# Kernel tuning notes

Hardware: AMD Instinct MI355X
Metric: run time of the kernel (lower is better)

The kernel has to match this reference:

```python
import jax, jax.numpy as jnp
import numpy as np

D = 128   # hidden_size
L = 50    # mailbox length (USER_MAX_LEN / ITEM_MAX_LEN)
NU = 8192 # num user nodes
NI = 8192 # num item nodes


def setup_inputs() -> dict:
    key = jax.random.key(0)
    ks = jax.random.split(key, 16)
    s = 0.05
    return {
        "user": jax.random.normal(ks[0], (NU, D), jnp.float32),
        "item": jax.random.normal(ks[1], (NI, D), jnp.float32),
        "W_user": jax.random.normal(ks[2], (D, D), jnp.float32) * s,
        "W_item": jax.random.normal(ks[3], (D, D), jnp.float32) * s,
        "agg_gate_user": jax.random.normal(ks[4], (2 * D, D), jnp.float32) * s,
        "agg_gate_item": jax.random.normal(ks[5], (2 * D, D), jnp.float32) * s,
        "update_user": jax.random.normal(ks[6], (2 * D, D), jnp.float32) * s,
        "update_item": jax.random.normal(ks[7], (2 * D, D), jnp.float32) * s,
        "user_date_emb": jax.random.normal(ks[8], (L, D), jnp.float32) * s,
        "user_date_emb_k": jax.random.normal(ks[9], (L, D), jnp.float32) * s,
        "item_date_emb": jax.random.normal(ks[10], (L, D), jnp.float32) * s,
        "item_date_emb_k": jax.random.normal(ks[11], (L, D), jnp.float32) * s,
        "user_nbr": jax.random.randint(ks[12], (NU, L), 0, NI, jnp.int64) if jax.config.jax_enable_x64 else jax.random.randint(ks[12], (NU, L), 0, NI, jnp.int32),
        "user_nbr_time": jax.random.randint(ks[13], (NU, L), 0, 1000000, jnp.int32),
        "item_nbr": jax.random.randint(ks[14], (NI, L), 0, NU, jnp.int32),
        "item_nbr_time": jax.random.randint(ks[15], (NI, L), 0, 1000000, jnp.int32),
    }


def _reduce(dst_h, src_mail, time, emb, emb_k, gate_W):
    # dst_h: [N,d], src_mail: [N,L,d], time: [N,L]
    # double argsort -> rank; reorder = L - rank - 1 (time-order position)
    order = jnp.argsort(jnp.argsort(time, axis=1), axis=1)
    reorder = time.shape[1] - order - 1                     # [N,L]
    scale = 1.0 / jnp.sqrt(jnp.asarray(dst_h.shape[-1], dst_h.dtype))
    # long-term attention with positional injection
    e = jnp.sum((emb[reorder] + src_mail) * dst_h[:, None, :], axis=-1) * scale
    alpha = jax.nn.softmax(e, axis=1)                       # [N,L]
    h_long = jnp.einsum('nl,nld->nd', alpha, src_mail + emb_k[reorder])
    # short-term attention against most-recent neighbor
    last = jnp.argmax(time, axis=1)                         # [N]
    last_emb = jnp.take_along_axis(src_mail, last[:, None, None], axis=1)  # [N,1,d]
    e1 = jnp.sum(last_emb * src_mail, axis=-1) * scale
    alpha1 = jax.nn.softmax(e1, axis=1)
    h_short = jnp.einsum('nl,nld->nd', alpha1, src_mail)
    return jnp.concatenate([h_long, h_short], axis=-1) @ gate_W  # [N,d]


def reference(user, item, W_user, W_item, agg_gate_user, agg_gate_item,
              update_user, update_item, user_date_emb, user_date_emb_k,
              item_date_emb, item_date_emb_k, user_nbr, user_nbr_time,
              item_nbr, item_nbr_time):
    # feat_drop/attn_drop are identity (eval mode)
    uh = user @ W_user   # [NU,d]
    ih = item @ W_item   # [NI,d]
    # user nodes aggregate item-neighbor mailboxes
    user_agg = _reduce(uh, ih[user_nbr], user_nbr_time,
                       user_date_emb, user_date_emb_k, agg_gate_user)
    # item nodes aggregate user-neighbor mailboxes
    item_agg = _reduce(ih, uh[item_nbr], item_nbr_time,
                       item_date_emb, item_date_emb_k, agg_gate_item)
    user_out = jnp.tanh(jnp.concatenate([user_agg, user], axis=-1) @ update_user)
    item_out = jnp.tanh(jnp.concatenate([item_agg, item], axis=-1) @ update_item)
    return user_out, item_out
```

## Files before the change

### kernel.cpp

```cpp
#include <hip/hip_runtime.h>
#include <math.h>

#define D 128
#define L 50
#define SCALE 0.08838834764831845f

using bf16x8 = __attribute__((ext_vector_type(8))) short;
using f32x4  = __attribute__((ext_vector_type(4))) float;

union FragU { bf16x8 f; uint2 u2[2]; uint4 u4; };

__device__ __forceinline__ unsigned f2bf(float x) {
    union { float f; unsigned u; } v; v.f = x;
    return (v.u + 0x7fffu + ((v.u >> 16) & 1u)) >> 16;
}
__device__ __forceinline__ float bflo(unsigned u) {
    union { unsigned u; float f; } v; v.u = u << 16; return v.f;
}
__device__ __forceinline__ float bfhi(unsigned u) {
    union { unsigned u; float f; } v; v.u = u & 0xffff0000u; return v.f;
}

__global__ __launch_bounds__(256) void prep_all_kernel(
    const float* __restrict__ Wu, const float* __restrict__ Wi,
    const float* __restrict__ ue, const float* __restrict__ ie,
    const float* __restrict__ gu, const float* __restrict__ gi,
    const float* __restrict__ uu, const float* __restrict__ ui,
    const float* __restrict__ uek, const float* __restrict__ iek,
    unsigned short* __restrict__ Bptu, unsigned short* __restrict__ Bpti,
    unsigned short* __restrict__ Btu, unsigned short* __restrict__ Bti)
{
    __shared__ float T[2][128];
    int b = blockIdx.x, t = threadIdx.x;
    if (b < 50) {
        int side = b / 25;
        int o = (b % 25) * 256 + t;
        int d = o / L, l = o % L;
        const float* W = side ? Wi : Wu;
        const float* E = side ? ie : ue;
        unsigned short* Bpt = side ? Bpti : Bptu;
        float a = 0.f;
        for (int k = 0; k < D; ++k) a += W[d * D + k] * E[l * D + k];
        Bpt[(128 + l) * 128 + d] = (unsigned short)f2bf(a);
    } else if (b < 306) {
        int bb = b - 50;
        int side = bb / 128;
        int o = (bb % 128) * 256 + t;
        int r = o >> 7, c = o & 127;
        const float* G = side ? gi : gu;
        const float* U = side ? ui : uu;
        unsigned short* Bt = side ? Bti : Btu;
        float a = 0.f;
        for (int k = 0; k < D; ++k) a += G[r * D + k] * U[k * D + c];
        Bt[c * 448 + r] = (unsigned short)f2bf(a);
    } else if (b < 434) {
        int bb = b - 306;
        int side = bb >> 6;
        int o = (bb & 63) * 256 + t;
        int r = o >> 7, c = o & 127;
        const float* U = side ? ui : uu;
        unsigned short* Bt = side ? Bti : Btu;
        Bt[c * 448 + 320 + r] = (unsigned short)f2bf(U[(128 + r) * D + c]);
        if (r < 14) Bt[c * 448 + 306 + r] = 0;
    } else if (b < 562) {
        int bb = b - 434;
        int side = bb >> 6;
        int o = (bb & 63) * 256 + t;
        int k = o >> 7, c = o & 127;
        const float* W = side ? Wi : Wu;
        unsigned short* Bpt = side ? Bpti : Bptu;
        Bpt[c * 128 + k] = (unsigned short)f2bf(W[k * D + c]);
    } else if (b < 564) {
        int side = b - 562;
        unsigned short* Bpt = side ? Bpti : Bptu;
        for (int j = 0; j < 7; ++j)
            Bpt[178 * 128 + t * 7 + j] = 0;
    } else {
        int bb = b - 564;
        int side = bb / 25;
        int ro = (bb % 25) * 2;
        const float* EK = side ? iek : uek;
        const float* G  = side ? gi : gu;
        const float* U  = side ? ui : uu;
        unsigned short* Bt = side ? Bti : Btu;
        int r = t >> 7, c = t & 127;
        float a = 0.f;
        for (int k = 0; k < D; ++k) a += EK[(ro + r) * D + k] * G[k * D + c];
        T[r][c] = a;
        __syncthreads();
        float e = 0.f;
        for (int j = 0; j < D; ++j) e += T[r][j] * U[j * D + c];
        Bt[c * 448 + 256 + ro + r] = (unsigned short)f2bf(e);
    }
}

__global__ __launch_bounds__(256) void proj_mfma(
    const float* __restrict__ Xu, const float* __restrict__ Xi,
    const unsigned* __restrict__ Bptu32, const unsigned* __restrict__ Bpti32,
    unsigned* __restrict__ h32, float* __restrict__ eproj,
    unsigned* __restrict__ A32, int NU)
{
    __shared__ __align__(16) unsigned Bs[192 * 68];
    int t = threadIdx.x;
    int nb = blockIdx.x * 32;
    const float* X = (nb < NU) ? Xu : Xi;
    int xoff = (nb < NU) ? 0 : NU;
    const unsigned* Bt = (nb < NU) ? Bptu32 : Bpti32;
    int wave = t >> 6, lane = t & 63;
    int m16 = lane & 15, quad = lane >> 4;

    #pragma unroll
    for (int i = 0; i < 12; ++i) {
        int idx = t + i * 256;
        int c = idx >> 4, q = idx & 15;
        uint4 v = *(const uint4*)&Bt[(size_t)c * 64 + q * 4];
        *(uint4*)&Bs[c * 68 + q * 4] = v;
    }
    __syncthreads();

    f32x4 acc[2][3];
    for (int i = 0; i < 2; ++i)
        for (int j = 0; j < 3; ++j) acc[i][j] = (f32x4){0.f, 0.f, 0.f, 0.f};

    #pragma unroll
    for (int kc = 0; kc < 4; ++kc) {
        FragU a[2];
        #pragma unroll
        for (int mi = 0; mi < 2; ++mi) {
            int row = nb + mi * 16 + m16;
            const float* src = &X[(size_t)(row - xoff) * D + kc * 32 + quad * 8];
            float4 v0 = *(const float4*)&src[0];
            float4 v1 = *(const float4*)&src[4];
            uint4 pk;
            pk.x = f2bf(v0.x) | (f2bf(v0.y) << 16);
            pk.y = f2bf(v0.z) | (f2bf(v0.w) << 16);
            pk.z = f2bf(v1.x) | (f2bf(v1.y) << 16);
            pk.w = f2bf(v1.z) | (f2bf(v1.w) << 16);
            a[mi].u4 = pk;
            if (wave == 0)
                *(uint4*)&A32[(size_t)row * 224 + 160 + kc * 16 + quad * 4] = pk;
        }
        #pragma unroll
        for (int ni = 0; ni < 3; ++ni) {
            bf16x8 bb = *(const bf16x8*)&Bs[(wave * 48 + ni * 16 + m16) * 68 + kc * 16 + quad * 4];
            acc[0][ni] = __builtin_amdgcn_mfma_f32_16x16x32_bf16(a[0].f, bb, acc[0][ni], 0, 0, 0);
            acc[1][ni] = __builtin_amdgcn_mfma_f32_16x16x32_bf16(a[1].f, bb, acc[1][ni], 0, 0, 0);
        }
    }
    #pragma unroll
    for (int mi = 0; mi < 2; ++mi)
        #pragma unroll
        for (int ni = 0; ni < 3; ++ni) {
            int col = wave * 48 + ni * 16 + m16;
            #pragma unroll
            for (int r = 0; r < 4; ++r) {
                float me = acc[mi][ni][r];
                float pr = __shfl_xor(me, 1);
                int row = nb + mi * 16 + quad * 4 + r;
                if (col < 128) {
                    if (!(lane & 1))
                        h32[(size_t)row * 64 + (col >> 1)] = f2bf(me) | (f2bf(pr) << 16);
                } else if (col < 178) {
                    eproj[(size_t)row * L + (col - 128)] = me;
                }
            }
        }
}

__global__ __launch_bounds__(256) void agg_kernel(
    const unsigned* __restrict__ h32, const float* __restrict__ eproj,
    const int* __restrict__ unbr, const int* __restrict__ untime,
    const int* __restrict__ inbr, const int* __restrict__ intime,
    unsigned* __restrict__ A32, int NU, int NI)
{
    __shared__ unsigned smail[2][L * 66];
    __shared__ unsigned shb[2][64];
    __shared__ float se2[2][2][64];
    __shared__ float salpha[2][L], salpha1[2][L];
    __shared__ int stime[2][L], sreorder[2][L], snbr[2][L], slast[2];

    int tb = threadIdx.x;
    int sub = tb >> 7;
    int t = tb & 127;
    int g = blockIdx.x * 2 + sub;
    int wave = t >> 6, lane = t & 63;
    int m16 = lane & 15, quad = lane >> 4;

    const unsigned* mail; const int* nbrp; const int* timp;
    if (g < NU) { mail = h32 + (size_t)NU * 64; nbrp = unbr + (size_t)g * L;        timp = untime + (size_t)g * L; }
    else        { mail = h32;                   nbrp = inbr + (size_t)(g - NU) * L; timp = intime + (size_t)(g - NU) * L; }

    if (t < 64) shb[sub][t] = h32[(size_t)g * 64 + t];
    if (t < L) { stime[sub][t] = timp[t]; snbr[sub][t] = nbrp[t]; }
    __syncthreads();

    if (t < L) {
        int ti = stime[sub][t]; int rank = 0; bool firstmax = true;
        for (int j = 0; j < L; ++j) {
            int tj = stime[sub][j];
            rank += (tj < ti) || (tj == ti && j < t);
            firstmax = firstmax && ((tj < ti) || (tj == ti && j >= t));
        }
        sreorder[sub][t] = L - 1 - rank;
        if (firstmax) slast[sub] = t;
    }
    {
        int q = t >> 5, p = t & 31;
        #pragma unroll
        for (int i = 0; i < 13; ++i) {
            int l = i * 4 + q;
            if (l < L) {
                uint2 v = *(const uint2*)&mail[(size_t)snbr[sub][l] * 64 + p * 2];
                *(uint2*)&smail[sub][l * 66 + 2 * p] = v;
            }
        }
    }
    __syncthreads();

    {
        const unsigned* bptr = (m16 == 1) ? &smail[sub][slast[sub] * 66]
                                          : &shb[sub][0];
        int s0 = wave * 32 + m16;  if (s0 > 49) s0 = 49;
        int s1 = wave * 32 + 16 + m16;  if (s1 > 49) s1 = 49;
        const unsigned* a0p = &smail[sub][s0 * 66];
        const unsigned* a1p = &smail[sub][s1 * 66];
        f32x4 d0 = {0.f, 0.f, 0.f, 0.f}, d1 = {0.f, 0.f, 0.f, 0.f};
        #pragma unroll
        for (int kc = 0; kc < 4; ++kc) {
            int off = kc * 16 + quad * 4;
            FragU bf_, af0, af1;
            bf_.u2[0] = *(const uint2*)&bptr[off];
            bf_.u2[1] = *(const uint2*)&bptr[off + 2];
            af0.u2[0] = *(const uint2*)&a0p[off];
            af0.u2[1] = *(const uint2*)&a0p[off + 2];
            af1.u2[0] = *(const uint2*)&a1p[off];
            af1.u2[1] = *(const uint2*)&a1p[off + 2];
            d0 = __builtin_amdgcn_mfma_f32_16x16x32_bf16(af0.f, bf_.f, d0, 0, 0, 0);
            d1 = __builtin_amdgcn_mfma_f32_16x16x32_bf16(af1.f, bf_.f, d1, 0, 0, 0);
        }
        if (m16 < 2) {
            #pragma unroll
            for (int r = 0; r < 4; ++r) {
                se2[sub][m16][wave * 32 + quad * 4 + r]      = d0[r];
                se2[sub][m16][wave * 32 + 16 + quad * 4 + r] = d1[r];
            }
        }
    }
    __syncthreads();

    float sc = -1e30f;
    if (lane < L) {
        sc = (wave == 0)
           ? (se2[sub][0][lane] + eproj[(size_t)g * L + sreorder[sub][lane]]) * SCALE
           : se2[sub][1][lane] * SCALE;
    }
    float mx = sc;
    for (int off = 32; off; off >>= 1) mx = fmaxf(mx, __shfl_xor(mx, off));
    float ex = (lane < L) ? expf(sc - mx) : 0.f;
    float sm = ex;
    for (int off = 32; off; off >>= 1) sm += __shfl_xor(sm, off);
    float al = ex / sm;
    if (lane < L) { if (wave == 0) salpha[sub][lane] = al; else salpha1[sub][lane] = al; }
    __syncthreads();

    {
        const float* alp = wave ? salpha1[sub] : salpha[sub];
        const unsigned* base = &smail[sub][lane];
        float ax = 0.f, ay = 0.f;
        for (int l = 0; l < L; ++l) {
            unsigned u = base[l * 66];
            float a = alp[l];
            ax += a * bflo(u);
            ay += a * bfhi(u);
        }
        A32[(size_t)g * 224 + wave * 64 + lane] = f2bf(ax) | (f2bf(ay) << 16);
    }
    if (t >= 64 && t < 96) A32[(size_t)g * 224 + 128 + (t - 64)] = 0u;
    __syncthreads();
    if (t < L) {
        ((unsigned short*)A32)[(size_t)g * 448 + 256 + sreorder[sub][t]] =
            (unsigned short)f2bf(salpha[sub][t]);
    }
}

__global__ __launch_bounds__(256) void gemm_out_mfma(
    const unsigned* __restrict__ A32,
    const unsigned* __restrict__ Btu32, const unsigned* __restrict__ Bti32,
    float* __restrict__ out, int NU)
{
    __shared__ __align__(16) unsigned Bs[64 * 228];
    int t = threadIdx.x;
    int rowblk = blockIdx.x >> 1, half = blockIdx.x & 1;
    int nb = rowblk * 128;
    const unsigned* Bt = (nb < NU) ? Btu32 : Bti32;
    int wave = t >> 6, lane = t & 63;
    int m16 = lane & 15, quad = lane >> 4;

    #pragma unroll
    for (int i = 0; i < 14; ++i) {
        int idx = t + i * 256;
        int n = idx / 56, q = idx - n * 56;
        uint4 v = *(const uint4*)&Bt[(size_t)(half * 64 + n) * 224 + q * 4];
        *(uint4*)&Bs[n * 228 + q * 4] = v;
    }
    __syncthreads();

    #pragma unroll
    for (int j = 0; j < 2; ++j) {
        int mrow0 = nb + (wave * 2 + j) * 16;
        f32x4 acc[4] = {{0.f,0.f,0.f,0.f},{0.f,0.f,0.f,0.f},
                        {0.f,0.f,0.f,0.f},{0.f,0.f,0.f,0.f}};
        for (int kc = 0; kc < 14; ++kc) {
            FragU af;
            af.u4 = *(const uint4*)&A32[(size_t)(mrow0 + m16) * 224 + kc * 16 + quad * 4];
            #pragma unroll
            for (int ni = 0; ni < 4; ++ni) {
                bf16x8 bf = *(const bf16x8*)&Bs[(ni * 16 + m16) * 228 + kc * 16 + quad * 4];
                acc[ni] = __builtin_amdgcn_mfma_f32_16x16x32_bf16(af.f, bf, acc[ni], 0, 0, 0);
            }
        }
        #pragma unroll
        for (int ni = 0; ni < 4; ++ni)
            #pragma unroll
            for (int r = 0; r < 4; ++r) {
                int row = mrow0 + quad * 4 + r;
                int col = half * 64 + ni * 16 + m16;
                out[(size_t)row * D + col] = tanhf(acc[ni][r]);
            }
    }
}

extern "C" void kernel_launch(void* const* d_in, const int* in_sizes, int n_in,
                              void* d_out, int out_size, void* d_ws, size_t ws_size,
                              hipStream_t stream) {
    const float* user   = (const float*)d_in[0];
    const float* item   = (const float*)d_in[1];
    const float* Wu     = (const float*)d_in[2];
    const float* Wi     = (const float*)d_in[3];
    const float* gate_u = (const float*)d_in[4];
    const float* gate_i = (const float*)d_in[5];
    const float* upd_u  = (const float*)d_in[6];
    const float* upd_i  = (const float*)d_in[7];
    const float* uemb   = (const float*)d_in[8];
    const float* uembk  = (const float*)d_in[9];
    const float* iemb   = (const float*)d_in[10];
    const float* iembk  = (const float*)d_in[11];
    const int*   unbr   = (const int*)d_in[12];
    const int*   untime = (const int*)d_in[13];
    const int*   inbr   = (const int*)d_in[14];
    const int*   intime = (const int*)d_in[15];

    int NU = in_sizes[0] / D;
    int NI = in_sizes[1] / D;
    int N  = NU + NI;

    float* eproj  = (float*)d_ws;
    unsigned* h32   = (unsigned*)(eproj + (size_t)N * L);
    unsigned* A32   = h32 + (size_t)N * 64;
    unsigned* Btu32 = A32 + (size_t)N * 224;
    unsigned* Bti32 = Btu32 + 128 * 224;
    unsigned* Bptu32 = Bti32 + 128 * 224;
    unsigned* Bpti32 = Bptu32 + 192 * 64;

    prep_all_kernel<<<614, 256, 0, stream>>>(Wu, Wi, uemb, iemb, gate_u, gate_i,
                                             upd_u, upd_i, uembk, iembk,
                                             (unsigned short*)Bptu32,
                                             (unsigned short*)Bpti32,
                                             (unsigned short*)Btu32,
                                             (unsigned short*)Bti32);
    proj_mfma<<<N / 32, 256, 0, stream>>>(user, item, Bptu32, Bpti32,
                                          h32, eproj, A32, NU);
    agg_kernel<<<N / 2, 256, 0, stream>>>(h32, eproj, unbr, untime, inbr,
                                          intime, A32, NU, NI);
    gemm_out_mfma<<<N / 64, 256, 0, stream>>>(A32, Btu32, Bti32,
                                              (float*)d_out, NU);
}
```

Baseline: 172.1 us.

## Fuse four stages into one persistent cooperative kernel with grid syncs

Merges the prep, projection, aggregation and output-GEMM kernels into a single persistent cooperative kernel. Blocks loop over work items and a grid.sync separates each stage, which removes three kernel launches and the gaps between them. The projection and output GEMM no longer stage B in shared memory and read it directly from global memory/cache. The projection tile is also halved to 16 rows per work item. Grid size is capped at 768 blocks, which limits parallelism in the agg stage. Host-side attribute and occupancy queries now run on every call, and the old four-kernel path is kept as a fallback.

```diff
diff --git a/kernel.cpp b/kernel.cpp
--- a/kernel.cpp
+++ b/kernel.cpp
@@ -1,5 +1,8 @@
 #include <hip/hip_runtime.h>
+#include <hip/hip_cooperative_groups.h>
 #include <math.h>
+
+namespace cg = cooperative_groups;
 
 #define D 128
 #define L 50
@@ -21,24 +24,31 @@
     union { unsigned u; float f; } v; v.u = u & 0xffff0000u; return v.f;
 }
 
-__global__ __launch_bounds__(256) void prep_all_kernel(
-    const float* __restrict__ Wu, const float* __restrict__ Wi,
-    const float* __restrict__ ue, const float* __restrict__ ie,
-    const float* __restrict__ gu, const float* __restrict__ gi,
-    const float* __restrict__ uu, const float* __restrict__ ui,
-    const float* __restrict__ uek, const float* __restrict__ iek,
-    unsigned short* __restrict__ Bptu, unsigned short* __restrict__ Bpti,
-    unsigned short* __restrict__ Btu, unsigned short* __restrict__ Bti)
-{
-    __shared__ float T[2][128];
-    int b = blockIdx.x, t = threadIdx.x;
+struct AggShared {
+    unsigned smail[2][L * 66];
+    unsigned shb[2][64];
+    float se2[2][2][64];
+    float salpha[2][L], salpha1[2][L];
+    int stime[2][L], sreorder[2][L], snbr[2][L], slast[2];
+};
+struct PrepShared { float T[2][128]; };
+union SharedAll { AggShared agg; PrepShared prep; };
+
+__device__ __forceinline__ void prep_body(
+    int b, int t,
+    const float* Wu, const float* Wi, const float* ue, const float* ie,
+    const float* gu, const float* gi, const float* uu, const float* ui,
+    const float* uek, const float* iek,
+    unsigned* Bptu32, unsigned* Bpti32, unsigned* Btu32, unsigned* Bti32,
+    float T[2][128])
+{
     if (b < 50) {
         int side = b / 25;
         int o = (b % 25) * 256 + t;
         int d = o / L, l = o % L;
         const float* W = side ? Wi : Wu;
         const float* E = side ? ie : ue;
-        unsigned short* Bpt = side ? Bpti : Bptu;
+        unsigned short* Bpt = (unsigned short*)(side ? Bpti32 : Bptu32);
         float a = 0.f;
         for (int k = 0; k < D; ++k) a += W[d * D + k] * E[l * D + k];
         Bpt[(128 + l) * 128 + d] = (unsigned short)f2bf(a);
@@ -49,7 +59,7 @@
         int r = o >> 7, c = o & 127;
         const float* G = side ? gi : gu;
         const float* U = side ? ui : uu;
-        unsigned short* Bt = side ? Bti : Btu;
+        unsigned short* Bt = (unsigned short*)(side ? Bti32 : Btu32);
         float a = 0.f;
         for (int k = 0; k < D; ++k) a += G[r * D + k] * U[k * D + c];
         Bt[c * 448 + r] = (unsigned short)f2bf(a);
@@ -59,7 +69,7 @@
         int o = (bb & 63) * 256 + t;
         int r = o >> 7, c = o & 127;
         const float* U = side ? ui : uu;
-        unsigned short* Bt = side ? Bti : Btu;
+        unsigned short* Bt = (unsigned short*)(side ? Bti32 : Btu32);
         Bt[c * 448 + 320 + r] = (unsigned short)f2bf(U[(128 + r) * D + c]);
         if (r < 14) Bt[c * 448 + 306 + r] = 0;
     } else if (b < 562) {
@@ -68,11 +78,11 @@
         int o = (bb & 63) * 256 + t;
         int k = o >> 7, c = o & 127;
         const float* W = side ? Wi : Wu;
-        unsigned short* Bpt = side ? Bpti : Bptu;
+        unsigned short* Bpt = (unsigned short*)(side ? Bpti32 : Bptu32);
         Bpt[c * 128 + k] = (unsigned short)f2bf(W[k * D + c]);
     } else if (b < 564) {
         int side = b - 562;
-        unsigned short* Bpt = side ? Bpti : Bptu;
+        unsigned short* Bpt = (unsigned short*)(side ? Bpti32 : Bptu32);
         for (int j = 0; j < 7; ++j)
             Bpt[178 * 128 + t * 7 + j] = 0;
     } else {
@@ -82,7 +92,7 @@
         const float* EK = side ? iek : uek;
         const float* G  = side ? gi : gu;
         const float* U  = side ? ui : uu;
-        unsigned short* Bt = side ? Bti : Btu;
+        unsigned short* Bt = (unsigned short*)(side ? Bti32 : Btu32);
         int r = t >> 7, c = t & 127;
         float a = 0.f;
         for (int k = 0; k < D; ++k) a += EK[(ro + r) * D + k] * G[k * D + c];
@@ -91,143 +101,116 @@
         float e = 0.f;
         for (int j = 0; j < D; ++j) e += T[r][j] * U[j * D + c];
         Bt[c * 448 + 256 + ro + r] = (unsigned short)f2bf(e);
-    }
-}
-
-__global__ __launch_bounds__(256) void proj_mfma(
-    const float* __restrict__ Xu, const float* __restrict__ Xi,
-    const unsigned* __restrict__ Bptu32, const unsigned* __restrict__ Bpti32,
-    unsigned* __restrict__ h32, float* __restrict__ eproj,
-    unsigned* __restrict__ A32, int NU)
-{
-    __shared__ __align__(16) unsigned Bs[192 * 68];
-    int t = threadIdx.x;
-    int nb = blockIdx.x * 32;
-    const float* X = (nb < NU) ? Xu : Xi;
+        __syncthreads();
+    }
+}
+
+__device__ __forceinline__ void proj_body(
+    int w, int t, const float* user, const float* item,
+    const unsigned* Bptu32, const unsigned* Bpti32,
+    unsigned* h32, float* eproj, unsigned* A32, int NU)
+{
+    int wave = t >> 6, lane = t & 63;
+    int m16 = lane & 15, quad = lane >> 4;
+    int nb = w * 16;
+    const float* X = (nb < NU) ? user : item;
     int xoff = (nb < NU) ? 0 : NU;
     const unsigned* Bt = (nb < NU) ? Bptu32 : Bpti32;
-    int wave = t >> 6, lane = t & 63;
-    int m16 = lane & 15, quad = lane >> 4;
-
-    #pragma unroll
-    for (int i = 0; i < 12; ++i) {
-        int idx = t + i * 256;
-        int c = idx >> 4, q = idx & 15;
-        uint4 v = *(const uint4*)&Bt[(size_t)c * 64 + q * 4];
-        *(uint4*)&Bs[c * 68 + q * 4] = v;
-    }
-    __syncthreads();
-
-    f32x4 acc[2][3];
-    for (int i = 0; i < 2; ++i)
-        for (int j = 0; j < 3; ++j) acc[i][j] = (f32x4){0.f, 0.f, 0.f, 0.f};
-
+
+    f32x4 acc[3] = {{0.f,0.f,0.f,0.f},{0.f,0.f,0.f,0.f},{0.f,0.f,0.f,0.f}};
     #pragma unroll
     for (int kc = 0; kc < 4; ++kc) {
-        FragU a[2];
-        #pragma unroll
-        for (int mi = 0; mi < 2; ++mi) {
-            int row = nb + mi * 16 + m16;
-            const float* src = &X[(size_t)(row - xoff) * D + kc * 32 + quad * 8];
-            float4 v0 = *(const float4*)&src[0];
-            float4 v1 = *(const float4*)&src[4];
-            uint4 pk;
-            pk.x = f2bf(v0.x) | (f2bf(v0.y) << 16);
-            pk.y = f2bf(v0.z) | (f2bf(v0.w) << 16);
-            pk.z = f2bf(v1.x) | (f2bf(v1.y) << 16);
-            pk.w = f2bf(v1.z) | (f2bf(v1.w) << 16);
-            a[mi].u4 = pk;
-            if (wave == 0)
-                *(uint4*)&A32[(size_t)row * 224 + 160 + kc * 16 + quad * 4] = pk;
-        }
+        int row = nb + m16;
+        const float* src = &X[(size_t)(row - xoff) * D + kc * 32 + quad * 8];
+        float4 v0 = *(const float4*)&src[0];
+        float4 v1 = *(const float4*)&src[4];
+        FragU a;
+        a.u4.x = f2bf(v0.x) | (f2bf(v0.y) << 16);
+        a.u4.y = f2bf(v0.z) | (f2bf(v0.w) << 16);
+        a.u4.z = f2bf(v1.x) | (f2bf(v1.y) << 16);
+        a.u4.w = f2bf(v1.z) | (f2bf(v1.w) << 16);
+        if (wave == 0)
+            *(uint4*)&A32[(size_t)row * 224 + 160 + kc * 16 + quad * 4] = a.u4;
         #pragma unroll
         for (int ni = 0; ni < 3; ++ni) {
-            bf16x8 bb = *(const bf16x8*)&Bs[(wave * 48 + ni * 16 + m16) * 68 + kc * 16 + quad * 4];
-            acc[0][ni] = __builtin_amdgcn_mfma_f32_16x16x32_bf16(a[0].f, bb, acc[0][ni], 0, 0, 0);
-            acc[1][ni] = __builtin_amdgcn_mfma_f32_16x16x32_bf16(a[1].f, bb, acc[1][ni], 0, 0, 0);
+            int c = wave * 48 + ni * 16 + m16;
+            FragU bb;
+            bb.u4 = *(const uint4*)&Bt[(size_t)c * 64 + kc * 16 + quad * 4];
+            acc[ni] = __builtin_amdgcn_mfma_f32_16x16x32_bf16(a.f, bb.f, acc[ni], 0, 0, 0);
         }
     }
     #pragma unroll
-    for (int mi = 0; mi < 2; ++mi)
-        #pragma unroll
-        for (int ni = 0; ni < 3; ++ni) {
-            int col = wave * 48 + ni * 16 + m16;
-            #pragma unroll
-            for (int r = 0; r < 4; ++r) {
-                float me = acc[mi][ni][r];
-                float pr = __shfl_xor(me, 1);
-                int row = nb + mi * 16 + quad * 4 + r;
-                if (col < 128) {
-                    if (!(lane & 1))
-                        h32[(size_t)row * 64 + (col >> 1)] = f2bf(me) | (f2bf(pr) << 16);
-                } else if (col < 178) {
-                    eproj[(size_t)row * L + (col - 128)] = me;
-                }
+    for (int ni = 0; ni < 3; ++ni) {
+        int col = wave * 48 + ni * 16 + m16;
+        #pragma unroll
+        for (int r = 0; r < 4; ++r) {
+            float me = acc[ni][r];
+            float pr = __shfl_xor(me, 1);
+            int row = nb + quad * 4 + r;
+            if (col < 128) {
+                if (!(lane & 1))
+                    h32[(size_t)row * 64 + (col >> 1)] = f2bf(me) | (f2bf(pr) << 16);
+            } else if (col < 178) {
+                eproj[(size_t)row * L + (col - 128)] = me;
             }
         }
-}
-
-__global__ __launch_bounds__(256) void agg_kernel(
-    const unsigned* __restrict__ h32, const float* __restrict__ eproj,
-    const int* __restrict__ unbr, const int* __restrict__ untime,
-    const int* __restrict__ inbr, const int* __restrict__ intime,
-    unsigned* __restrict__ A32, int NU, int NI)
-{
-    __shared__ unsigned smail[2][L * 66];
-    __shared__ unsigned shb[2][64];
-    __shared__ float se2[2][2][64];
-    __shared__ float salpha[2][L], salpha1[2][L];
-    __shared__ int stime[2][L], sreorder[2][L], snbr[2][L], slast[2];
-
-    int tb = threadIdx.x;
+    }
+}
+
+__device__ __forceinline__ void agg_body(
+    int w, int tb, AggShared& sh,
+    const unsigned* h32, const float* eproj,
+    const int* unbr, const int* untime, const int* inbr, const int* intime,
+    unsigned* A32, int NU)
+{
     int sub = tb >> 7;
-    int t = tb & 127;
-    int g = blockIdx.x * 2 + sub;
-    int wave = t >> 6, lane = t & 63;
-    int m16 = lane & 15, quad = lane >> 4;
+    int ta = tb & 127;
+    int awave = ta >> 6, alane = ta & 63;
+    int am16 = alane & 15, aquad = alane >> 4;
+    int g = w * 2 + sub;
 
     const unsigned* mail; const int* nbrp; const int* timp;
     if (g < NU) { mail = h32 + (size_t)NU * 64; nbrp = unbr + (size_t)g * L;        timp = untime + (size_t)g * L; }
     else        { mail = h32;                   nbrp = inbr + (size_t)(g - NU) * L; timp = intime + (size_t)(g - NU) * L; }
 
-    if (t < 64) shb[sub][t] = h32[(size_t)g * 64 + t];
-    if (t < L) { stime[sub][t] = timp[t]; snbr[sub][t] = nbrp[t]; }
-    __syncthreads();
-
-    if (t < L) {
-        int ti = stime[sub][t]; int rank = 0; bool firstmax = true;
+    if (ta < 64) sh.shb[sub][ta] = h32[(size_t)g * 64 + ta];
+    if (ta < L) { sh.stime[sub][ta] = timp[ta]; sh.snbr[sub][ta] = nbrp[ta]; }
+    __syncthreads();
+
+    if (ta < L) {
+        int ti = sh.stime[sub][ta]; int rank = 0; bool firstmax = true;
         for (int j = 0; j < L; ++j) {
-            int tj = stime[sub][j];
-            rank += (tj < ti) || (tj == ti && j < t);
-            firstmax = firstmax && ((tj < ti) || (tj == ti && j >= t));
-        }
-        sreorder[sub][t] = L - 1 - rank;
-        if (firstmax) slast[sub] = t;
+            int tj = sh.stime[sub][j];
+            rank += (tj < ti) || (tj == ti && j < ta);
+            firstmax = firstmax && ((tj < ti) || (tj == ti && j >= ta));
+        }
+        sh.sreorder[sub][ta] = L - 1 - rank;
+        if (firstmax) sh.slast[sub] = ta;
     }
     {
-        int q = t >> 5, p = t & 31;
+        int q = ta >> 5, p = ta & 31;
         #pragma unroll
         for (int i = 0; i < 13; ++i) {
             int l = i * 4 + q;
             if (l < L) {
-                uint2 v = *(const uint2*)&mail[(size_t)snbr[sub][l] * 64 + p * 2];
-                *(uint2*)&smail[sub][l * 66 + 2 * p] = v;
+                uint2 v = *(const uint2*)&mail[(size_t)sh.snbr[sub][l] * 64 + p * 2];
+                *(uint2*)&sh.smail[sub][l * 66 + 2 * p] = v;
             }
         }
     }
     __syncthreads();
 
     {
-        const unsigned* bptr = (m16 == 1) ? &smail[sub][slast[sub] * 66]
-                                          : &shb[sub][0];
-        int s0 = wave * 32 + m16;  if (s0 > 49) s0 = 49;
-        int s1 = wave * 32 + 16 + m16;  if (s1 > 49) s1 = 49;
-        const unsigned* a0p = &smail[sub][s0 * 66];
-        const unsigned* a1p = &smail[sub][s1 * 66];
+        const unsigned* bptr = (am16 == 1) ? &sh.smail[sub][sh.slast[sub] * 66]
+                                           : &sh.shb[sub][0];
+        int s0 = awave * 32 + am16;       if (s0 > 49) s0 = 49;
+        int s1 = awave * 32 + 16 + am16;  if (s1 > 49) s1 = 49;
+        const unsigned* a0p = &sh.smail[sub][s0 * 66];
+        const unsigned* a1p = &sh.smail[sub][s1 * 66];
         f32x4 d0 = {0.f, 0.f, 0.f, 0.f}, d1 = {0.f, 0.f, 0.f, 0.f};
         #pragma unroll
         for (int kc = 0; kc < 4; ++kc) {
-            int off = kc * 16 + quad * 4;
+            int off = kc * 16 + aquad * 4;
             FragU bf_, af0, af1;
             bf_.u2[0] = *(const uint2*)&bptr[off];
             bf_.u2[1] = *(const uint2*)&bptr[off + 2];
@@ -238,34 +221,37 @@
             d0 = __builtin_amdgcn_mfma_f32_16x16x32_bf16(af0.f, bf_.f, d0, 0, 0, 0);
             d1 = __builtin_amdgcn_mfma_f32_16x16x32_bf16(af1.f, bf_.f, d1, 0, 0, 0);
         }
-        if (m16 < 2) {
+        if (am16 < 2) {
             #pragma unroll
             for (int r = 0; r < 4; ++r) {
-                se2[sub][m16][wave * 32 + quad * 4 + r]      = d0[r];
-                se2[sub][m16][wave * 32 + 16 + quad * 4 + r] = d1[r];
+                sh.se2[sub][am16][awave * 32 + aquad * 4 + r]      = d0[r];
+                sh.se2[sub][am16][awave * 32 + 16 + aquad * 4 + r] = d1[r];
             }
         }
     }
     __syncthreads();
 
     float sc = -1e30f;
-    if (lane < L) {
-        sc = (wave == 0)
-           ? (se2[sub][0][lane] + eproj[(size_t)g * L + sreorder[sub][lane]]) * SCALE
-           : se2[sub][1][lane] * SCALE;
+    if (alane < L) {
+        sc = (awave == 0)
+           ? (sh.se2[sub][0][alane] + eproj[(size_t)g * L + sh.sreorder[sub][alane]]) * SCALE
+           : sh.se2[sub][1][alane] * SCALE;
     }
     float mx = sc;
     for (int off = 32; off; off >>= 1) mx = fmaxf(mx, __shfl_xor(mx, off));
-    float ex = (lane < L) ? expf(sc - mx) : 0.f;
-    float sm = ex;
-    for (int off = 32; off; off >>= 1) sm += __shfl_xor(sm, off);
-    float al = ex / sm;
-    if (lane < L) { if (wave == 0) salpha[sub][lane] = al; else salpha1[sub][lane] = al; }
+    float ex = (alane < L) ? expf(sc - mx) : 0.f;
+    float smv = ex;
+    for (int off = 32; off; off >>= 1) smv += __shfl_xor(smv, off);
+    float al = ex / smv;
+    if (alane < L) {
+        if (awave == 0) sh.salpha[sub][alane] = al;
+        else            sh.salpha1[sub][alane] = al;
+    }
     __syncthreads();
 
     {
-        const float* alp = wave ? salpha1[sub] : salpha[sub];
-        const unsigned* base = &smail[sub][lane];
+        const float* alp = awave ? sh.salpha1[sub] : sh.salpha[sub];
+        const unsigned* base = &sh.smail[sub][alane];
         float ax = 0.f, ay = 0.f;
         for (int l = 0; l < L; ++l) {
             unsigned u = base[l * 66];
@@ -273,61 +259,136 @@
             ax += a * bflo(u);
             ay += a * bfhi(u);
         }
-        A32[(size_t)g * 224 + wave * 64 + lane] = f2bf(ax) | (f2bf(ay) << 16);
-    }
-    if (t >= 64 && t < 96) A32[(size_t)g * 224 + 128 + (t - 64)] = 0u;
-    __syncthreads();
-    if (t < L) {
-        ((unsigned short*)A32)[(size_t)g * 448 + 256 + sreorder[sub][t]] =
-            (unsigned short)f2bf(salpha[sub][t]);
-    }
-}
-
-__global__ __launch_bounds__(256) void gemm_out_mfma(
-    const unsigned* __restrict__ A32,
-    const unsigned* __restrict__ Btu32, const unsigned* __restrict__ Bti32,
-    float* __restrict__ out, int NU)
-{
-    __shared__ __align__(16) unsigned Bs[64 * 228];
-    int t = threadIdx.x;
-    int rowblk = blockIdx.x >> 1, half = blockIdx.x & 1;
+        A32[(size_t)g * 224 + awave * 64 + alane] = f2bf(ax) | (f2bf(ay) << 16);
+    }
+    if (ta >= 64 && ta < 96) A32[(size_t)g * 224 + 128 + (ta - 64)] = 0u;
+    __syncthreads();
+    if (ta < L) {
+        ((unsigned short*)A32)[(size_t)g * 448 + 256 + sh.sreorder[sub][ta]] =
+            (unsigned short)f2bf(sh.salpha[sub][ta]);
+    }
+    __syncthreads();
+}
+
+__device__ __forceinline__ void gemm_body(
+    int w, int t, const unsigned* A32,
+    const unsigned* Btu32, const unsigned* Bti32, float* out, int NU)
+{
+    int wave = t >> 6, lane = t & 63;
+    int m16 = lane & 15, quad = lane >> 4;
+    int rowblk = w >> 1, half = w & 1;
     int nb = rowblk * 128;
     const unsigned* Bt = (nb < NU) ? Btu32 : Bti32;
-    int wave = t >> 6, lane = t & 63;
-    int m16 = lane & 15, quad = lane >> 4;
-
+    int mr0 = nb + (wave * 2) * 16 + m16;
+    int mr1 = mr0 + 16;
+
+    f32x4 acc[2][4];
     #pragma unroll
-    for (int i = 0; i < 14; ++i) {
-        int idx = t + i * 256;
-        int n = idx / 56, q = idx - n * 56;
-        uint4 v = *(const uint4*)&Bt[(size_t)(half * 64 + n) * 224 + q * 4];
-        *(uint4*)&Bs[n * 228 + q * 4] = v;
-    }
-    __syncthreads();
-
+    for (int i = 0; i < 2; ++i)
+        #pragma unroll
+        for (int j = 0; j < 4; ++j) acc[i][j] = (f32x4){0.f, 0.f, 0.f, 0.f};
+
+    for (int kc = 0; kc < 14; ++kc) {
+        FragU a0, a1;
+        a0.u4 = *(const uint4*)&A32[(size_t)mr0 * 224 + kc * 16 + quad * 4];
+        a1.u4 = *(const uint4*)&A32[(size_t)mr1 * 224 + kc * 16 + quad * 4];
+        #pragma unroll
+        for (int ni = 0; ni < 4; ++ni) {
+            FragU bf;
+            bf.u4 = *(const uint4*)&Bt[(size_t)(half * 64 + ni * 16 + m16) * 224 + kc * 16 + quad * 4];
+            acc[0][ni] = __builtin_amdgcn_mfma_f32_16x16x32_bf16(a0.f, bf.f, acc[0][ni], 0, 0, 0);
+            acc[1][ni] = __builtin_amdgcn_mfma_f32_16x16x32_bf16(a1.f, bf.f, acc[1][ni], 0, 0, 0);
+        }
+    }
     #pragma unroll
     for (int j = 0; j < 2; ++j) {
         int mrow0 = nb + (wave * 2 + j) * 16;
-        f32x4 acc[4] = {{0.f,0.f,0.f,0.f},{0.f,0.f,0.f,0.f},
-                        {0.f,0.f,0.f,0.f},{0.f,0.f,0.f,0.f}};
-        for (int kc = 0; kc < 14; ++kc) {
-            FragU af;
-            af.u4 = *(const uint4*)&A32[(size_t)(mrow0 + m16) * 224 + kc * 16 + quad * 4];
-            #pragma unroll
-            for (int ni = 0; ni < 4; ++ni) {
-                bf16x8 bf = *(const bf16x8*)&Bs[(ni * 16 + m16) * 228 + kc * 16 + quad * 4];
-                acc[ni] = __builtin_amdgcn_mfma_f32_16x16x32_bf16(af.f, bf, acc[ni], 0, 0, 0);
-            }
-        }
         #pragma unroll
         for (int ni = 0; ni < 4; ++ni)
             #pragma unroll
             for (int r = 0; r < 4; ++r) {
                 int row = mrow0 + quad * 4 + r;
                 int col = half * 64 + ni * 16 + m16;
-                out[(size_t)row * D + col] = tanhf(acc[ni][r]);
+                out[(size_t)row * D + col] = tanhf(acc[j][ni][r]);
             }
     }
+}
+
+__global__ __launch_bounds__(256, 2) void mega_kernel(
+    const float* __restrict__ user, const float* __restrict__ item,
+    const float* __restrict__ Wu, const float* __restrict__ Wi,
+    const float* __restrict__ gu, const float* __restrict__ gi,
+    const float* __restrict__ uu, const float* __restrict__ ui,
+    const float* __restrict__ ue, const float* __restrict__ ie,
+    const float* __restrict__ uek, const float* __restrict__ iek,
+    const int* __restrict__ unbr, const int* __restrict__ untime,
+    const int* __restrict__ inbr, const int* __restrict__ intime,
+    float* __restrict__ eproj, unsigned* __restrict__ h32,
+    unsigned* __restrict__ A32,
+    unsigned* __restrict__ Btu32, unsigned* __restrict__ Bti32,
+    unsigned* __restrict__ Bptu32, unsigned* __restrict__ Bpti32,
+    float* __restrict__ out, int NU, int NI)
+{
+    __shared__ SharedAll sm;
+    cg::grid_group grid = cg::this_grid();
+    int t = threadIdx.x;
+    int N = NU + NI;
+
+    for (int b = blockIdx.x; b < 614; b += gridDim.x)
+        prep_body(b, t, Wu, Wi, ue, ie, gu, gi, uu, ui, uek, iek,
+                  Bptu32, Bpti32, Btu32, Bti32, sm.prep.T);
+    __threadfence();
+    grid.sync();
+
+    for (int w = blockIdx.x; w < N / 16; w += gridDim.x)
+        proj_body(w, t, user, item, Bptu32, Bpti32, h32, eproj, A32, NU);
+    __threadfence();
+    grid.sync();
+
+    for (int w = blockIdx.x; w < N / 2; w += gridDim.x)
+        agg_body(w, t, sm.agg, h32, eproj, unbr, untime, inbr, intime, A32, NU);
+    __threadfence();
+    grid.sync();
+
+    for (int w = blockIdx.x; w < N / 64; w += gridDim.x)
+        gemm_body(w, t, A32, Btu32, Bti32, out, NU);
+}
+
+__global__ __launch_bounds__(256) void prep_k(
+    const float* Wu, const float* Wi, const float* ue, const float* ie,
+    const float* gu, const float* gi, const float* uu, const float* ui,
+    const float* uek, const float* iek,
+    unsigned* Bptu32, unsigned* Bpti32, unsigned* Btu32, unsigned* Bti32)
+{
+    __shared__ float T[2][128];
+    prep_body(blockIdx.x, threadIdx.x, Wu, Wi, ue, ie, gu, gi, uu, ui,
+              uek, iek, Bptu32, Bpti32, Btu32, Bti32, T);
+}
+
+__global__ __launch_bounds__(256) void proj_k(
+    const float* user, const float* item,
+    const unsigned* Bptu32, const unsigned* Bpti32,
+    unsigned* h32, float* eproj, unsigned* A32, int NU)
+{
+    proj_body(blockIdx.x, threadIdx.x, user, item, Bptu32, Bpti32,
+              h32, eproj, A32, NU);
+}
+
+__global__ __launch_bounds__(256) void agg_k(
+    const unsigned* h32, const float* eproj,
+    const int* unbr, const int* untime, const int* inbr, const int* intime,
+    unsigned* A32, int NU)
+{
+    __shared__ AggShared sh;
+    agg_body(blockIdx.x, threadIdx.x, sh, h32, eproj, unbr, untime,
+             inbr, intime, A32, NU);
+}
+
+__global__ __launch_bounds__(256) void gemm_k(
+    const unsigned* A32, const unsigned* Btu32, const unsigned* Bti32,
+    float* out, int NU)
+{
+    gemm_body(blockIdx.x, threadIdx.x, A32, Btu32, Bti32, out, NU);
 }
 
 extern "C" void kernel_launch(void* const* d_in, const int* in_sizes, int n_in,
@@ -361,17 +422,38 @@
     unsigned* Bti32 = Btu32 + 128 * 224;
     unsigned* Bptu32 = Bti32 + 128 * 224;
     unsigned* Bpti32 = Bptu32 + 192 * 64;
-
-    prep_all_kernel<<<614, 256, 0, stream>>>(Wu, Wi, uemb, iemb, gate_u, gate_i,
-                                             upd_u, upd_i, uembk, iembk,
-                                             (unsigned short*)Bptu32,
-                                             (unsigned short*)Bpti32,
-                                             (unsigned short*)Btu32,
-                                             (unsigned short*)Bti32);
-    proj_mfma<<<N / 32, 256, 0, stream>>>(user, item, Bptu32, Bpti32,
-                                          h32, eproj, A32, NU);
-    agg_kernel<<<N / 2, 256, 0, stream>>>(h32, eproj, unbr, untime, inbr,
-                                          intime, A32, NU, NI);
-    gemm_out_mfma<<<N / 64, 256, 0, stream>>>(A32, Btu32, Bti32,
-                                              (float*)d_out, NU);
-}
+    float* out = (float*)d_out;
+
+    hipError_t rc = hipErrorUnknown;
+    int coop = 0, numCU = 0, maxBlk = 0, dev = 0;
+    (void)hipGetDevice(&dev);
+    (void)hipDeviceGetAttribute(&coop, hipDeviceAttributeCooperativeLaunch, dev);
+    (void)hipDeviceGetAttribute(&numCU, hipDeviceAttributeMultiprocessorCount, dev);
+    (void)hipOccupancyMaxActiveBlocksPerMultiprocessor(
+        &maxBlk, (const void*)mega_kernel, 256, 0);
+    if (coop && numCU > 0 && maxBlk > 0) {
+        int nblk = maxBlk * numCU;
+        if (nblk > 768) nblk = 768;
+        void* args[] = {
+            (void*)&user, (void*)&item, (void*)&Wu, (void*)&Wi,
+            (void*)&gate_u, (void*)&gate_i, (void*)&upd_u, (void*)&upd_i,
+            (void*)&uemb, (void*)&iemb, (void*)&uembk, (void*)&iembk,
+            (void*)&unbr, (void*)&untime, (void*)&inbr, (void*)&intime,
+            (void*)&eproj, (void*)&h32, (void*)&A32,
+            (void*)&Btu32, (void*)&Bti32, (void*)&Bptu32, (void*)&Bpti32,
+            (void*)&out, (void*)&NU, (void*)&NI
+        };
+        rc = hipLaunchCooperativeKernel((void*)mega_kernel, dim3(nblk),
+                                        dim3(256), args, 0, stream);
+    }
+    if (rc != hipSuccess) {
+        prep_k<<<614, 256, 0, stream>>>(Wu, Wi, uemb, iemb, gate_u, gate_i,
+                                        upd_u, upd_i, uembk, iembk,
+                                        Bptu32, Bpti32, Btu32, Bti32);
+        proj_k<<<N / 16, 256, 0, stream>>>(user, item, Bptu32, Bpti32,
+                                           h32, eproj, A32, NU);
+        agg_k<<<N / 2, 256, 0, stream>>>(h32, eproj, unbr, untime, inbr,
+                                         intime, A32, NU);
+        gemm_k<<<N / 64, 256, 0, stream>>>(A32, Btu32, Bti32, out, NU);
+    }
+}
```

Result: slower. 618.6 us (+259.4%).

## Split weight prep so the gate-matrix prep overlaps the projection kernel

Applied to the files above, without the earlier changes.

The prep kernel is split in two. Only the projection-weight blocks needed by the projection run first. The gate/update weight prep blocks are appended to the projection grid so they run alongside it, which removes one serial dependency stage. The projection kernel also drops its shared-memory staging of B, now handles 16 rows per block (twice as many blocks), and reads B fragments straight from global memory. The A32 zero-fill moves earlier in the aggregation kernel so one __syncthreads can be removed. The trade-off is more global/L2 traffic for B and more blocks.

```diff
diff --git a/kernel.cpp b/kernel.cpp
--- a/kernel.cpp
+++ b/kernel.cpp
@@ -21,24 +21,21 @@
     union { unsigned u; float f; } v; v.u = u & 0xffff0000u; return v.f;
 }
 
-__global__ __launch_bounds__(256) void prep_all_kernel(
-    const float* __restrict__ Wu, const float* __restrict__ Wi,
-    const float* __restrict__ ue, const float* __restrict__ ie,
-    const float* __restrict__ gu, const float* __restrict__ gi,
-    const float* __restrict__ uu, const float* __restrict__ ui,
-    const float* __restrict__ uek, const float* __restrict__ iek,
-    unsigned short* __restrict__ Bptu, unsigned short* __restrict__ Bpti,
-    unsigned short* __restrict__ Btu, unsigned short* __restrict__ Bti)
-{
-    __shared__ float T[2][128];
-    int b = blockIdx.x, t = threadIdx.x;
+__device__ __forceinline__ void prep_body(
+    int b, int t,
+    const float* Wu, const float* Wi, const float* ue, const float* ie,
+    const float* gu, const float* gi, const float* uu, const float* ui,
+    const float* uek, const float* iek,
+    unsigned* Bptu32, unsigned* Bpti32, unsigned* Btu32, unsigned* Bti32,
+    float T[2][128])
+{
     if (b < 50) {
         int side = b / 25;
         int o = (b % 25) * 256 + t;
         int d = o / L, l = o % L;
         const float* W = side ? Wi : Wu;
         const float* E = side ? ie : ue;
-        unsigned short* Bpt = side ? Bpti : Bptu;
+        unsigned short* Bpt = (unsigned short*)(side ? Bpti32 : Bptu32);
         float a = 0.f;
         for (int k = 0; k < D; ++k) a += W[d * D + k] * E[l * D + k];
         Bpt[(128 + l) * 128 + d] = (unsigned short)f2bf(a);
@@ -49,7 +46,7 @@
         int r = o >> 7, c = o & 127;
         const float* G = side ? gi : gu;
         const float* U = side ? ui : uu;
-        unsigned short* Bt = side ? Bti : Btu;
+        unsigned short* Bt = (unsigned short*)(side ? Bti32 : Btu32);
         float a = 0.f;
         for (int k = 0; k < D; ++k) a += G[r * D + k] * U[k * D + c];
         Bt[c * 448 + r] = (unsigned short)f2bf(a);
@@ -59,7 +56,7 @@
         int o = (bb & 63) * 256 + t;
         int r = o >> 7, c = o & 127;
         const float* U = side ? ui : uu;
-        unsigned short* Bt = side ? Bti : Btu;
+        unsigned short* Bt = (unsigned short*)(side ? Bti32 : Btu32);
         Bt[c * 448 + 320 + r] = (unsigned short)f2bf(U[(128 + r) * D + c]);
         if (r < 14) Bt[c * 448 + 306 + r] = 0;
     } else if (b < 562) {
@@ -68,11 +65,11 @@
         int o = (bb & 63) * 256 + t;
         int k = o >> 7, c = o & 127;
         const float* W = side ? Wi : Wu;
-        unsigned short* Bpt = side ? Bpti : Bptu;
+        unsigned short* Bpt = (unsigned short*)(side ? Bpti32 : Bptu32);
         Bpt[c * 128 + k] = (unsigned short)f2bf(W[k * D + c]);
     } else if (b < 564) {
         int side = b - 562;
-        unsigned short* Bpt = side ? Bpti : Bptu;
+        unsigned short* Bpt = (unsigned short*)(side ? Bpti32 : Bptu32);
         for (int j = 0; j < 7; ++j)
             Bpt[178 * 128 + t * 7 + j] = 0;
     } else {
@@ -82,7 +79,7 @@
         const float* EK = side ? iek : uek;
         const float* G  = side ? gi : gu;
         const float* U  = side ? ui : uu;
-        unsigned short* Bt = side ? Bti : Btu;
+        unsigned short* Bt = (unsigned short*)(side ? Bti32 : Btu32);
         int r = t >> 7, c = t & 127;
         float a = 0.f;
         for (int k = 0; k < D; ++k) a += EK[(ro + r) * D + k] * G[k * D + c];
@@ -91,87 +88,103 @@
         float e = 0.f;
         for (int j = 0; j < D; ++j) e += T[r][j] * U[j * D + c];
         Bt[c * 448 + 256 + ro + r] = (unsigned short)f2bf(e);
-    }
-}
-
-__global__ __launch_bounds__(256) void proj_mfma(
-    const float* __restrict__ Xu, const float* __restrict__ Xi,
-    const unsigned* __restrict__ Bptu32, const unsigned* __restrict__ Bpti32,
-    unsigned* __restrict__ h32, float* __restrict__ eproj,
-    unsigned* __restrict__ A32, int NU)
-{
-    __shared__ __align__(16) unsigned Bs[192 * 68];
-    int t = threadIdx.x;
-    int nb = blockIdx.x * 32;
-    const float* X = (nb < NU) ? Xu : Xi;
+        __syncthreads();
+    }
+}
+
+__device__ __forceinline__ void proj_body(
+    int w, int t, const float* user, const float* item,
+    const unsigned* Bptu32, const unsigned* Bpti32,
+    unsigned* h32, float* eproj, unsigned* A32, int NU)
+{
+    int wave = t >> 6, lane = t & 63;
+    int m16 = lane & 15, quad = lane >> 4;
+    int nb = w * 16;
+    const float* X = (nb < NU) ? user : item;
     int xoff = (nb < NU) ? 0 : NU;
     const unsigned* Bt = (nb < NU) ? Bptu32 : Bpti32;
-    int wave = t >> 6, lane = t & 63;
-    int m16 = lane & 15, quad = lane >> 4;
-
-    #pragma unroll
-    for (int i = 0; i < 12; ++i) {
-        int idx = t + i * 256;
-        int c = idx >> 4, q = idx & 15;
-        uint4 v = *(const uint4*)&Bt[(size_t)c * 64 + q * 4];
-        *(uint4*)&Bs[c * 68 + q * 4] = v;
-    }
-    __syncthreads();
-
-    f32x4 acc[2][3];
-    for (int i = 0; i < 2; ++i)
-        for (int j = 0; j < 3; ++j) acc[i][j] = (f32x4){0.f, 0.f, 0.f, 0.f};
-
+
+    f32x4 acc[3] = {{0.f,0.f,0.f,0.f},{0.f,0.f,0.f,0.f},{0.f,0.f,0.f,0.f}};
     #pragma unroll
     for (int kc = 0; kc < 4; ++kc) {
-        FragU a[2];
-        #pragma unroll
-        for (int mi = 0; mi < 2; ++mi) {
-            int row = nb + mi * 16 + m16;
-            const float* src = &X[(size_t)(row - xoff) * D + kc * 32 + quad * 8];
-            float4 v0 = *(const float4*)&src[0];
-            float4 v1 = *(const float4*)&src[4];
-            uint4 pk;
-            pk.x = f2bf(v0.x) | (f2bf(v0.y) << 16);
-            pk.y = f2bf(v0.z) | (f2bf(v0.w) << 16);
-            pk.z = f2bf(v1.x) | (f2bf(v1.y) << 16);
-            pk.w = f2bf(v1.z) | (f2bf(v1.w) << 16);
-            a[mi].u4 = pk;
-            if (wave == 0)
-                *(uint4*)&A32[(size_t)row * 224 + 160 + kc * 16 + quad * 4] = pk;
-        }
+        int row = nb + m16;
+        const float* src = &X[(size_t)(row - xoff) * D + kc * 32 + quad * 8];
+        float4 v0 = *(const float4*)&src[0];
+        float4 v1 = *(const float4*)&src[4];
+        FragU a;
+        a.u4.x = f2bf(v0.x) | (f2bf(v0.y) << 16);
+        a.u4.y = f2bf(v0.z) | (f2bf(v0.w) << 16);
+        a.u4.z = f2bf(v1.x) | (f2bf(v1.y) << 16);
+        a.u4.w = f2bf(v1.z) | (f2bf(v1.w) << 16);
+        if (wave == 0)
+            *(uint4*)&A32[(size_t)row * 224 + 160 + kc * 16 + quad * 4] = a.u4;
         #pragma unroll
         for (int ni = 0; ni < 3; ++ni) {
-            bf16x8 bb = *(const bf16x8*)&Bs[(wave * 48 + ni * 16 + m16) * 68 + kc * 16 + quad * 4];
-            acc[0][ni] = __builtin_amdgcn_mfma_f32_16x16x32_bf16(a[0].f, bb, acc[0][ni], 0, 0, 0);
-            acc[1][ni] = __builtin_amdgcn_mfma_f32_16x16x32_bf16(a[1].f, bb, acc[1][ni], 0, 0, 0);
+            int c = wave * 48 + ni * 16 + m16;
+            FragU bb;
+            bb.u4 = *(const uint4*)&Bt[(size_t)c * 64 + kc * 16 + quad * 4];
+            acc[ni] = __builtin_amdgcn_mfma_f32_16x16x32_bf16(a.f, bb.f, acc[ni], 0, 0, 0);
         }
     }
     #pragma unroll
-    for (int mi = 0; mi < 2; ++mi)
-        #pragma unroll
-        for (int ni = 0; ni < 3; ++ni) {
-            int col = wave * 48 + ni * 16 + m16;
-            #pragma unroll
-            for (int r = 0; r < 4; ++r) {
-                float me = acc[mi][ni][r];
-                float pr = __shfl_xor(me, 1);
-                int row = nb + mi * 16 + quad * 4 + r;
-                if (col < 128) {
-                    if (!(lane & 1))
-                        h32[(size_t)row * 64 + (col >> 1)] = f2bf(me) | (f2bf(pr) << 16);
-                } else if (col < 178) {
-                    eproj[(size_t)row * L + (col - 128)] = me;
-                }
-            }
-        }
-}
-
-__global__ __launch_bounds__(256) void agg_kernel(
+    for (int ni = 0; ni < 3; ++ni) {
+        int col = wave * 48 + ni * 16 + m16;
+        #pragma unroll
+        for (int r = 0; r < 4; ++r) {
+            float me = acc[ni][r];
+            float pr = __shfl_xor(me, 1);
+            int row = nb + quad * 4 + r;
+            if (col < 128) {
+                if (!(lane & 1))
+                    h32[(size_t)row * 64 + (col >> 1)] = f2bf(me) | (f2bf(pr) << 16);
+            } else if (col < 178) {
+                eproj[(size_t)row * L + (col - 128)] = me;
+            }
+        }
+    }
+}
+
+__global__ __launch_bounds__(256) void prepA_k(
+    const float* Wu, const float* Wi, const float* ue, const float* ie,
+    const float* gu, const float* gi, const float* uu, const float* ui,
+    const float* uek, const float* iek,
+    unsigned* Bptu32, unsigned* Bpti32, unsigned* Btu32, unsigned* Bti32)
+{
+    __shared__ float T[2][128];
+    int b = blockIdx.x;
+    int borig = (b < 50) ? b : b + 384;
+    prep_body(borig, threadIdx.x, Wu, Wi, ue, ie, gu, gi, uu, ui,
+              uek, iek, Bptu32, Bpti32, Btu32, Bti32, T);
+}
+
+__global__ __launch_bounds__(256) void proj_prepB_k(
+    const float* user, const float* item,
+    const float* Wu, const float* Wi, const float* ue, const float* ie,
+    const float* gu, const float* gi, const float* uu, const float* ui,
+    const float* uek, const float* iek,
+    const unsigned* Bptu32, const unsigned* Bpti32,
+    unsigned* h32, float* eproj, unsigned* A32,
+    unsigned* Btu32, unsigned* Bti32, int NU, int nproj)
+{
+    __shared__ float T[2][128];
+    int b = blockIdx.x;
+    if (b < nproj) {
+        proj_body(b, threadIdx.x, user, item, Bptu32, Bpti32,
+                  h32, eproj, A32, NU);
+    } else {
+        int bb = b - nproj;
+        int borig = (bb < 384) ? bb + 50 : bb - 384 + 564;
+        prep_body(borig, threadIdx.x, Wu, Wi, ue, ie, gu, gi, uu, ui,
+                  uek, iek, (unsigned*)Bptu32, (unsigned*)Bpti32,
+                  Btu32, Bti32, T);
+    }
+}
+
+__global__ __launch_bounds__(256) void agg_k(
     const unsigned* __restrict__ h32, const float* __restrict__ eproj,
     const int* __restrict__ unbr, const int* __restrict__ untime,
     const int* __restrict__ inbr, const int* __restrict__ intime,
-    unsigned* __restrict__ A32, int NU, int NI)
+    unsigned* __restrict__ A32, int NU)
 {
     __shared__ unsigned smail[2][L * 66];
     __shared__ unsigned shb[2][64];
@@ -192,6 +205,7 @@
 
     if (t < 64) shb[sub][t] = h32[(size_t)g * 64 + t];
     if (t < L) { stime[sub][t] = timp[t]; snbr[sub][t] = nbrp[t]; }
+    if (t >= 64 && t < 96) A32[(size_t)g * 224 + 128 + (t - 64)] = 0u;
     __syncthreads();
 
     if (t < L) {
@@ -220,7 +234,7 @@
     {
         const unsigned* bptr = (m16 == 1) ? &smail[sub][slast[sub] * 66]
                                           : &shb[sub][0];
-        int s0 = wave * 32 + m16;  if (s0 > 49) s0 = 49;
+        int s0 = wave * 32 + m16;       if (s0 > 49) s0 = 49;
         int s1 = wave * 32 + 16 + m16;  if (s1 > 49) s1 = 49;
         const unsigned* a0p = &smail[sub][s0 * 66];
         const unsigned* a1p = &smail[sub][s1 * 66];
@@ -275,15 +289,13 @@
         }
         A32[(size_t)g * 224 + wave * 64 + lane] = f2bf(ax) | (f2bf(ay) << 16);
     }
-    if (t >= 64 && t < 96) A32[(size_t)g * 224 + 128 + (t - 64)] = 0u;
-    __syncthreads();
     if (t < L) {
         ((unsigned short*)A32)[(size_t)g * 448 + 256 + sreorder[sub][t]] =
             (unsigned short)f2bf(salpha[sub][t]);
     }
 }
 
-__global__ __launch_bounds__(256) void gemm_out_mfma(
+__global__ __launch_bounds__(256) void gemm_k(
     const unsigned* __restrict__ A32,
     const unsigned* __restrict__ Btu32, const unsigned* __restrict__ Bti32,
     float* __restrict__ out, int NU)
@@ -353,6 +365,7 @@
     int NU = in_sizes[0] / D;
     int NI = in_sizes[1] / D;
     int N  = NU + NI;
+    int nproj = N / 16;
 
     float* eproj  = (float*)d_ws;
     unsigned* h32   = (unsigned*)(eproj + (size_t)N * L);
@@ -361,17 +374,16 @@
     unsigned* Bti32 = Btu32 + 128 * 224;
     unsigned* Bptu32 = Bti32 + 128 * 224;
     unsigned* Bpti32 = Bptu32 + 192 * 64;
-
-    prep_all_kernel<<<614, 256, 0, stream>>>(Wu, Wi, uemb, iemb, gate_u, gate_i,
-                                             upd_u, upd_i, uembk, iembk,
-                                             (unsigned short*)Bptu32,
-                                             (unsigned short*)Bpti32,
-                                             (unsigned short*)Btu32,
-                                             (unsigned short*)Bti32);
-    proj_mfma<<<N / 32, 256, 0, stream>>>(user, item, Bptu32, Bpti32,
-                                          h32, eproj, A32, NU);
-    agg_kernel<<<N / 2, 256, 0, stream>>>(h32, eproj, unbr, untime, inbr,
-                                          intime, A32, NU, NI);
-    gemm_out_mfma<<<N / 64, 256, 0, stream>>>(A32, Btu32, Bti32,
-                                              (float*)d_out, NU);
-}
+    float* out = (float*)d_out;
+
+    prepA_k<<<180, 256, 0, stream>>>(Wu, Wi, uemb, iemb, gate_u, gate_i,
+                                     upd_u, upd_i, uembk, iembk,
+                                     Bptu32, Bpti32, Btu32, Bti32);
+    proj_prepB_k<<<nproj + 434, 256, 0, stream>>>(
+        user, item, Wu, Wi, uemb, iemb, gate_u, gate_i, upd_u, upd_i,
+        uembk, iembk, Bptu32, Bpti32, h32, eproj, A32, Btu32, Bti32,
+        NU, nproj);
+    agg_k<<<N / 2, 256, 0, stream>>>(h32, eproj, unbr, untime, inbr,
+                                     intime, A32, NU);
+    gemm_k<<<N / 64, 256, 0, stream>>>(A32, Btu32, Bti32, out, NU);
+}
```

After: 177.8 us. 3.3% more time.
